# Performance work log

Hardware: AMD Instinct MI355X
Metric: run time of the kernel (lower is better)

## Reference

```python
import jax, jax.numpy as jnp
import numpy as np

EARLY = 1.5
GAP = 3.0
LATE = 2.0

def setup_inputs() -> dict:
    key = jax.random.key(0)
    k1, k2 = jax.random.split(key)
    N = 20_000_000
    inputs = jax.random.normal(k1, (N, 1), dtype=jnp.float32)
    targets = jax.random.normal(k2, (N, 1), dtype=jnp.float32)
    return {"inputs": inputs, "targets": targets}

def reference(inputs, targets):
    # train=True path: diff = targets - inputs, row-wise weight on column 0
    diff = targets - inputs                      # [N, 1]
    weight = jnp.where(diff >= GAP, EARLY,
             jnp.where(diff < 0.0, LATE, 1.0)).astype(diff.dtype)
    sq = (diff * weight) ** 2
    return jnp.sqrt(jnp.mean(sq))
```

## Files before the change

kernel.cpp:

```cpp
#include <hip/hip_runtime.h>
#include <math.h>

#define EARLY 1.5f
#define GAP   3.0f
#define LATE  2.0f

#define NBLOCKS 2048
#define NTHREADS 256

__device__ __forceinline__ float term(float a, float b) {
    float d = b - a;
    float w = (d >= GAP) ? EARLY : ((d < 0.0f) ? LATE : 1.0f);
    float t = d * w;
    return t * t;
}

__global__ __launch_bounds__(NTHREADS) void rmse_partial_kernel(
    const float* __restrict__ in, const float* __restrict__ tg,
    float* __restrict__ partial, int n)
{
    const int n4 = n >> 2;
    const float4* __restrict__ in4 = (const float4*)in;
    const float4* __restrict__ tg4 = (const float4*)tg;

    float acc = 0.0f;
    int idx = blockIdx.x * blockDim.x + threadIdx.x;
    int stride = gridDim.x * blockDim.x;

    for (int i = idx; i < n4; i += stride) {
        float4 a = in4[i];
        float4 b = tg4[i];
        acc += term(a.x, b.x);
        acc += term(a.y, b.y);
        acc += term(a.z, b.z);
        acc += term(a.w, b.w);
    }
    for (int i = (n4 << 2) + idx; i < n; i += stride) {
        acc += term(in[i], tg[i]);
    }

    #pragma unroll
    for (int off = 32; off > 0; off >>= 1)
        acc += __shfl_down(acc, off, 64);

    __shared__ float smem[NTHREADS / 64];
    int lane = threadIdx.x & 63;
    int wid  = threadIdx.x >> 6;
    if (lane == 0) smem[wid] = acc;
    __syncthreads();

    if (threadIdx.x == 0) {
        float t = 0.0f;
        #pragma unroll
        for (int w = 0; w < NTHREADS / 64; ++w) t += smem[w];
        partial[blockIdx.x] = t;
    }
}

__global__ __launch_bounds__(NTHREADS) void rmse_final_kernel(
    const float* __restrict__ partial, int nb,
    float* __restrict__ out, float invN)
{
    float acc = 0.0f;
    for (int i = threadIdx.x; i < nb; i += blockDim.x)
        acc += partial[i];

    #pragma unroll
    for (int off = 32; off > 0; off >>= 1)
        acc += __shfl_down(acc, off, 64);

    __shared__ float smem[NTHREADS / 64];
    int lane = threadIdx.x & 63;
    int wid  = threadIdx.x >> 6;
    if (lane == 0) smem[wid] = acc;
    __syncthreads();

    if (threadIdx.x == 0) {
        float t = 0.0f;
        #pragma unroll
        for (int w = 0; w < NTHREADS / 64; ++w) t += smem[w];
        out[0] = sqrtf(t * invN);
    }
}

extern "C" void kernel_launch(void* const* d_in, const int* in_sizes, int n_in,
                              void* d_out, int out_size, void* d_ws, size_t ws_size,
                              hipStream_t stream) {
    const float* inputs  = (const float*)d_in[0];
    const float* targets = (const float*)d_in[1];
    float* out = (float*)d_out;
    float* partial = (float*)d_ws;
    int n = in_sizes[0];

    rmse_partial_kernel<<<NBLOCKS, NTHREADS, 0, stream>>>(inputs, targets, partial, n);
    rmse_final_kernel<<<1, NTHREADS, 0, stream>>>(partial, NBLOCKS, out, 1.0f / (float)n);
}
```

Before: 32.17 us.

## Fuse final reduction via last-block atomic counter and unroll loads four-deep

Merges the two-kernel reduction into one kernel in which the last block to finish, detected through an atomic counter, sums the per-block partials and writes the square root. It also unrolls the grid-stride loop four-deep with independent accumulators to keep more loads in flight. The second kernel launch goes away, but a hipMemsetAsync is added to reset the counter, so the number of stream operations stays the same. Correctness depends on threadfence ordering and on the workspace having room for the counter.

Result: slower. 98.48 us (+206.2%).

```diff
diff --git a/kernel.cpp b/kernel.cpp
--- a/kernel.cpp
+++ b/kernel.cpp
@@ -7,6 +7,7 @@
 
 #define NBLOCKS 2048
 #define NTHREADS 256
+#define NWAVES (NTHREADS / 64)
 
 __device__ __forceinline__ float term(float a, float b) {
     float d = b - a;
@@ -15,71 +16,81 @@
     return t * t;
 }
 
-__global__ __launch_bounds__(NTHREADS) void rmse_partial_kernel(
+__device__ __forceinline__ float term4(float4 a, float4 b) {
+    return term(a.x, b.x) + term(a.y, b.y) + term(a.z, b.z) + term(a.w, b.w);
+}
+
+__global__ __launch_bounds__(NTHREADS) void rmse_fused_kernel(
     const float* __restrict__ in, const float* __restrict__ tg,
-    float* __restrict__ partial, int n)
+    float* __restrict__ out, float* __restrict__ partial,
+    unsigned int* __restrict__ counter, int n, float invN)
 {
     const int n4 = n >> 2;
     const float4* __restrict__ in4 = (const float4*)in;
     const float4* __restrict__ tg4 = (const float4*)tg;
 
-    float acc = 0.0f;
-    int idx = blockIdx.x * blockDim.x + threadIdx.x;
-    int stride = gridDim.x * blockDim.x;
+    const int tid = blockIdx.x * NTHREADS + threadIdx.x;
+    const int stride = NBLOCKS * NTHREADS;
 
-    for (int i = idx; i < n4; i += stride) {
-        float4 a = in4[i];
-        float4 b = tg4[i];
-        acc += term(a.x, b.x);
-        acc += term(a.y, b.y);
-        acc += term(a.z, b.z);
-        acc += term(a.w, b.w);
+    float acc0 = 0.f, acc1 = 0.f, acc2 = 0.f, acc3 = 0.f;
+    int i = tid;
+    for (; i + 3 * stride < n4; i += 4 * stride) {
+        float4 a0 = in4[i];              float4 b0 = tg4[i];
+        float4 a1 = in4[i + stride];     float4 b1 = tg4[i + stride];
+        float4 a2 = in4[i + 2 * stride]; float4 b2 = tg4[i + 2 * stride];
+        float4 a3 = in4[i + 3 * stride]; float4 b3 = tg4[i + 3 * stride];
+        acc0 += term4(a0, b0);
+        acc1 += term4(a1, b1);
+        acc2 += term4(a2, b2);
+        acc3 += term4(a3, b3);
     }
-    for (int i = (n4 << 2) + idx; i < n; i += stride) {
-        acc += term(in[i], tg[i]);
-    }
+    for (; i < n4; i += stride)
+        acc0 += term4(in4[i], tg4[i]);
+    for (int j = (n4 << 2) + tid; j < n; j += stride)
+        acc1 += term(in[j], tg[j]);
+
+    float acc = (acc0 + acc1) + (acc2 + acc3);
 
     #pragma unroll
     for (int off = 32; off > 0; off >>= 1)
         acc += __shfl_down(acc, off, 64);
 
-    __shared__ float smem[NTHREADS / 64];
-    int lane = threadIdx.x & 63;
-    int wid  = threadIdx.x >> 6;
+    __shared__ float smem[NWAVES];
+    const int lane = threadIdx.x & 63;
+    const int wid  = threadIdx.x >> 6;
     if (lane == 0) smem[wid] = acc;
     __syncthreads();
 
+    __shared__ bool is_last;
     if (threadIdx.x == 0) {
-        float t = 0.0f;
+        float t = 0.f;
         #pragma unroll
-        for (int w = 0; w < NTHREADS / 64; ++w) t += smem[w];
+        for (int w = 0; w < NWAVES; ++w) t += smem[w];
         partial[blockIdx.x] = t;
+        __threadfence();
+        unsigned int old = atomicAdd(counter, 1u);
+        is_last = (old == (unsigned int)(gridDim.x - 1));
     }
-}
-
-__global__ __launch_bounds__(NTHREADS) void rmse_final_kernel(
-    const float* __restrict__ partial, int nb,
-    float* __restrict__ out, float invN)
-{
-    float acc = 0.0f;
-    for (int i = threadIdx.x; i < nb; i += blockDim.x)
-        acc += partial[i];
-
-    #pragma unroll
-    for (int off = 32; off > 0; off >>= 1)
-        acc += __shfl_down(acc, off, 64);
-
-    __shared__ float smem[NTHREADS / 64];
-    int lane = threadIdx.x & 63;
-    int wid  = threadIdx.x >> 6;
-    if (lane == 0) smem[wid] = acc;
     __syncthreads();
 
-    if (threadIdx.x == 0) {
-        float t = 0.0f;
+    if (is_last) {
+        __threadfence();
+        float t = 0.f;
+        for (int p = threadIdx.x; p < NBLOCKS; p += NTHREADS) {
+            t += __hip_atomic_load(&partial[p], __ATOMIC_RELAXED,
+                                   __HIP_MEMORY_SCOPE_AGENT);
+        }
         #pragma unroll
-        for (int w = 0; w < NTHREADS / 64; ++w) t += smem[w];
-        out[0] = sqrtf(t * invN);
+        for (int off = 32; off > 0; off >>= 1)
+            t += __shfl_down(t, off, 64);
+        if (lane == 0) smem[wid] = t;
+        __syncthreads();
+        if (threadIdx.x == 0) {
+            float s = 0.f;
+            #pragma unroll
+            for (int w = 0; w < NWAVES; ++w) s += smem[w];
+            out[0] = sqrtf(s * invN);
+        }
     }
 }
 
@@ -90,8 +101,10 @@
     const float* targets = (const float*)d_in[1];
     float* out = (float*)d_out;
     float* partial = (float*)d_ws;
+    unsigned int* counter = (unsigned int*)((char*)d_ws + NBLOCKS * sizeof(float));
     int n = in_sizes[0];
 
-    rmse_partial_kernel<<<NBLOCKS, NTHREADS, 0, stream>>>(inputs, targets, partial, n);
-    rmse_final_kernel<<<1, NTHREADS, 0, stream>>>(partial, NBLOCKS, out, 1.0f / (float)n);
+    hipMemsetAsync(counter, 0, sizeof(unsigned int), stream);
+    rmse_fused_kernel<<<NBLOCKS, NTHREADS, 0, stream>>>(
+        inputs, targets, out, partial, counter, n, 1.0f / (float)n);
 }
```
